# Performance work log

Hardware: AMD Instinct MI355X
Metric: run time of the kernel (lower is better)

## Reference

```python
import jax, jax.numpy as jnp
import numpy as np

N_NODES = 50000
N_EDGES = 800000
IN_FEATS = 32
OUT_FEATS = 64
GRIDSIZE = 8


def setup_inputs() -> dict:
    key = jax.random.key(0)
    k1, k2, k3, k4 = jax.random.split(key, 4)
    x = jax.random.normal(k1, (N_NODES, IN_FEATS), dtype=jnp.float32)
    src = jax.random.randint(k2, (N_EDGES,), 0, N_NODES, dtype=jnp.int32)
    dst = jax.random.randint(k3, (N_EDGES,), 0, N_NODES, dtype=jnp.int32)
    scale = 1.0 / (np.sqrt(IN_FEATS) * np.sqrt(GRIDSIZE))
    fouriercoeffs = jax.random.normal(
        k4, (2, OUT_FEATS, IN_FEATS, GRIDSIZE), dtype=jnp.float32) * scale
    bias = jnp.zeros((OUT_FEATS,), dtype=jnp.float32)
    return {"x": x, "src": src, "dst": dst,
            "fouriercoeffs": fouriercoeffs, "bias": bias}


def reference(x, src, dst, fouriercoeffs, bias):
    # Per-edge source features: [E, in]
    src_feat = x[src]
    # Fourier frequencies k = 1..gridsize: [grid]
    k = jnp.arange(1, GRIDSIZE + 1, dtype=src_feat.dtype)
    # kx: [E, in, grid]
    kx = src_feat[:, :, None] * k[None, None, :]
    cos_kx = jnp.cos(kx)
    sin_kx = jnp.sin(kx)
    # Messages: einsum 'dbik,djik->bj' with d=2 stack of (cos, sin)
    m = (jnp.einsum('eik,jik->ej', cos_kx, fouriercoeffs[0])
         + jnp.einsum('eik,jik->ej', sin_kx, fouriercoeffs[1]))
    # Sum-scatter messages onto destination nodes: [N, out]
    h = jax.ops.segment_sum(m, dst, num_segments=N_NODES)
    return h + bias[None, :]
```

## Files before the change

kernel.cpp:

```cpp
#include <hip/hip_runtime.h>
#include <hip/hip_bf16.h>
#include <math.h>

#define IN_FEATS  32
#define OUT_FEATS 64
#define KDIM      512
#define NPB       64
#define ELLW      64

typedef __attribute__((ext_vector_type(8))) short bf16x8;
typedef __attribute__((ext_vector_type(4))) float f32x4;

static __device__ __forceinline__ unsigned short f2bf(float f) {
    unsigned u = __builtin_bit_cast(unsigned, f);
    return (unsigned short)((u + 0x7fffu + ((u >> 16) & 1u)) >> 16);
}
static __device__ __forceinline__ float bf2f(unsigned short h) {
    return __builtin_bit_cast(float, (unsigned)h << 16);
}

__global__ __launch_bounds__(256) void fkan_node_msg(
    const float* __restrict__ x,
    const float* __restrict__ fc,
    unsigned short* __restrict__ M,
    int* __restrict__ cnt,
    int n_nodes)
{
    __shared__ __align__(16) short phi[NPB * KDIM];
    const int tid  = threadIdx.x;
    const int lane = tid & 63;
    const int wid  = tid >> 6;
    const int nbase = blockIdx.x * NPB;

    if (tid < NPB) {
        const int n = nbase + tid;
        if (n < n_nodes) cnt[n] = 0;
    }

    const int j0   = wid * 16;
    const int brow = j0 + (lane & 15);
    const int kofs = 8 * (lane >> 4);
    bf16x8 bfrag[16];
#pragma unroll
    for (int ks = 0; ks < 16; ++ks) {
        const int K  = ks * 32 + kofs;
        const int b  = K >> 8;
        const int ik = K & 255;
        const float* p = fc + ((size_t)(b * OUT_FEATS + brow) * 256 + ik);
        const float4 f0 = *(const float4*)p;
        const float4 f1 = *(const float4*)(p + 4);
        bf16x8 t;
        t[0] = (short)f2bf(f0.x); t[1] = (short)f2bf(f0.y);
        t[2] = (short)f2bf(f0.z); t[3] = (short)f2bf(f0.w);
        t[4] = (short)f2bf(f1.x); t[5] = (short)f2bf(f1.y);
        t[6] = (short)f2bf(f1.z); t[7] = (short)f2bf(f1.w);
        bfrag[ks] = t;
    }

    {
        const int node = tid >> 2;
        const int q    = tid & 3;
        const int n    = nbase + node;
        char* rowp = (char*)phi + node * 1024;
        const int sw = (node & 7) << 4;
        float xv[8];
        if (n < n_nodes) {
            const float4 a = *(const float4*)(x + (size_t)n * 32 + q * 8);
            const float4 b = *(const float4*)(x + (size_t)n * 32 + q * 8 + 4);
            xv[0]=a.x; xv[1]=a.y; xv[2]=a.z; xv[3]=a.w;
            xv[4]=b.x; xv[5]=b.y; xv[6]=b.z; xv[7]=b.w;
        } else {
#pragma unroll
            for (int u = 0; u < 8; ++u) xv[u] = 0.f;
        }
#pragma unroll
        for (int u = 0; u < 8; ++u) {
            const int i = q * 8 + u;
            const float f  = xv[u] * 0.15915494309189535f;
            const float fr = f - floorf(f);
            const float s1 = __builtin_amdgcn_sinf(fr);
            const float c1 = __builtin_amdgcn_cosf(fr);
            const float twoc = 2.f * c1;
            float cAm = 1.f, sAm = 0.f, cA = c1, sA = s1;
            int pcv[4], psv[4];
#pragma unroll
            for (int p = 0; p < 4; ++p) {
                const float cB = twoc * cA - cAm;
                const float sB = twoc * sA - sAm;
                pcv[p] = (int)(((unsigned)f2bf(cB) << 16) | f2bf(cA));
                psv[p] = (int)(((unsigned)f2bf(sB) << 16) | f2bf(sA));
                const float cN = twoc * cB - cA;
                const float sN = twoc * sB - sA;
                cAm = cB; sAm = sB; cA = cN; sA = sN;
            }
            int4 vc; vc.x = pcv[0]; vc.y = pcv[1]; vc.z = pcv[2]; vc.w = pcv[3];
            int4 vs; vs.x = psv[0]; vs.y = psv[1]; vs.z = psv[2]; vs.w = psv[3];
            *(int4*)(rowp + ((i * 16) ^ sw))       = vc;
            *(int4*)(rowp + ((512 + i * 16) ^ sw)) = vs;
        }
    }
    __syncthreads();

    f32x4 acc[4] = {{0.f,0.f,0.f,0.f},{0.f,0.f,0.f,0.f},
                    {0.f,0.f,0.f,0.f},{0.f,0.f,0.f,0.f}};
    const int arow = lane & 15;
    const int sw   = (arow & 7) << 4;
    const int kbyt = 16 * (lane >> 4);
#pragma unroll
    for (int ks = 0; ks < 16; ++ks) {
#pragma unroll
        for (int nt = 0; nt < 4; ++nt) {
            const int row = nt * 16 + arow;
            const bf16x8 afrag = *(const bf16x8*)
                ((const char*)phi + row * 1024 + ((ks * 64 + kbyt) ^ sw));
            acc[nt] = __builtin_amdgcn_mfma_f32_16x16x32_bf16(
                afrag, bfrag[ks], acc[nt], 0, 0, 0);
        }
    }

    const int rem = n_nodes - nbase;
#pragma unroll
    for (int nt = 0; nt < 4; ++nt) {
        const int rbase = nt * 16 + (lane >> 4) * 4;
#pragma unroll
        for (int r = 0; r < 4; ++r) {
            const int node = rbase + r;
            if (node < rem)
                M[(size_t)(nbase + node) * OUT_FEATS + j0 + (lane & 15)] =
                    f2bf(acc[nt][r]);
        }
    }
}

__global__ __launch_bounds__(256) void fkan_fill(
    const int* __restrict__ src, const int* __restrict__ dst,
    int* __restrict__ cnt, unsigned short* __restrict__ ebuf,
    int n_edges, int n8)
{
    const int r    = blockIdx.x & 7;
    const int slab = blockIdx.x >> 3;
    const int e0   = (slab * 256 + threadIdx.x) * 4;
    if (e0 >= n_edges) return;
    const int lim = r * n8;
    if (e0 + 3 < n_edges) {
        const int4 d4 = *(const int4*)(dst + e0);
        if ((unsigned)(d4.x - lim) < (unsigned)n8) {
            const int pos = atomicAdd(&cnt[d4.x], 1);
            if (pos < ELLW) ebuf[(size_t)d4.x * ELLW + pos] = (unsigned short)src[e0 + 0];
        }
        if ((unsigned)(d4.y - lim) < (unsigned)n8) {
            const int pos = atomicAdd(&cnt[d4.y], 1);
            if (pos < ELLW) ebuf[(size_t)d4.y * ELLW + pos] = (unsigned short)src[e0 + 1];
        }
        if ((unsigned)(d4.z - lim) < (unsigned)n8) {
            const int pos = atomicAdd(&cnt[d4.z], 1);
            if (pos < ELLW) ebuf[(size_t)d4.z * ELLW + pos] = (unsigned short)src[e0 + 2];
        }
        if ((unsigned)(d4.w - lim) < (unsigned)n8) {
            const int pos = atomicAdd(&cnt[d4.w], 1);
            if (pos < ELLW) ebuf[(size_t)d4.w * ELLW + pos] = (unsigned short)src[e0 + 3];
        }
    } else {
        for (int e = e0; e < n_edges; ++e) {
            const int d = dst[e];
            if ((unsigned)(d - lim) < (unsigned)n8) {
                const int pos = atomicAdd(&cnt[d], 1);
                if (pos < ELLW) ebuf[(size_t)d * ELLW + pos] = (unsigned short)src[e];
            }
        }
    }
}

__global__ __launch_bounds__(256) void fkan_gather(
    const int* __restrict__ cnt, const unsigned short* __restrict__ ebuf,
    const unsigned short* __restrict__ M, const float* __restrict__ bias,
    float* __restrict__ out, int n_nodes)
{
    const int tid  = threadIdx.x;
    const int lane = tid & 63;
    const int node = blockIdx.x * 8 + (tid >> 6) * 2 + (lane >> 5);
    if (node >= n_nodes) return;
    const int len = min(cnt[node], ELLW);
    const unsigned short* row = ebuf + (size_t)node * ELLW;
    const int l32  = lane & 31;
    const int sub  = l32 >> 3;
    const int colb = (l32 & 7) * 8;
    float acc[8] = {0.f,0.f,0.f,0.f,0.f,0.f,0.f,0.f};
    const bf16x8 vz = {0,0,0,0,0,0,0,0};
    const unsigned ones = 0x3F803F80u;
    for (int e = 0; e < len; e += 8) {
        const int eeA = e + sub;
        const int eeB = e + 4 + sub;
        const bool pA = eeA < len;
        const bool pB = eeB < len;
        const int sA = pA ? row[eeA] : 0;
        const int sB = pB ? row[eeB] : 0;
        const bf16x8 vA = pA ? *(const bf16x8*)(M + (size_t)sA * OUT_FEATS + colb) : vz;
        const bf16x8 vB = pB ? *(const bf16x8*)(M + (size_t)sB * OUT_FEATS + colb) : vz;
        const uint4 ua = __builtin_bit_cast(uint4, vA);
        const uint4 ub = __builtin_bit_cast(uint4, vB);
        const unsigned uaw[4] = {ua.x, ua.y, ua.z, ua.w};
        const unsigned ubw[4] = {ub.x, ub.y, ub.z, ub.w};
#pragma unroll
        for (int w = 0; w < 4; ++w) {
            const unsigned lo = __builtin_amdgcn_perm(uaw[w], ubw[w], 0x05040100u);
            const unsigned hi = __builtin_amdgcn_perm(uaw[w], ubw[w], 0x07060302u);
            asm("v_dot2_f32_bf16 %0, %1, %2, %0"
                : "+v"(acc[2 * w]) : "v"(lo), "v"(ones));
            asm("v_dot2_f32_bf16 %0, %1, %2, %0"
                : "+v"(acc[2 * w + 1]) : "v"(hi), "v"(ones));
        }
    }
#pragma unroll
    for (int m = 8; m <= 16; m <<= 1) {
#pragma unroll
        for (int c = 0; c < 8; ++c) acc[c] += __shfl_xor(acc[c], m);
    }
    if (sub == 0) {
        const float4 b0 = *(const float4*)(bias + colb);
        const float4 b1 = *(const float4*)(bias + colb + 4);
        float4 o0; o0.x = acc[0] + b0.x; o0.y = acc[1] + b0.y;
                   o0.z = acc[2] + b0.z; o0.w = acc[3] + b0.w;
        float4 o1; o1.x = acc[4] + b1.x; o1.y = acc[5] + b1.y;
                   o1.z = acc[6] + b1.z; o1.w = acc[7] + b1.w;
        *(float4*)(out + (size_t)node * OUT_FEATS + colb)     = o0;
        *(float4*)(out + (size_t)node * OUT_FEATS + colb + 4) = o1;
    }
}

extern "C" void kernel_launch(void* const* d_in, const int* in_sizes, int n_in,
                              void* d_out, int out_size, void* d_ws, size_t ws_size,
                              hipStream_t stream)
{
    const float* x    = (const float*)d_in[0];
    const int*   src  = (const int*)d_in[1];
    const int*   dst  = (const int*)d_in[2];
    const float* fc   = (const float*)d_in[3];
    const float* bias = (const float*)d_in[4];
    float* out = (float*)d_out;

    const int n_nodes = in_sizes[0] / IN_FEATS;
    const int n_edges = in_sizes[1];
    const int n8      = (n_nodes + 7) / 8;

    char* ws = (char*)d_ws;
    unsigned short* M    = (unsigned short*)ws;
    unsigned short* ebuf = (unsigned short*)(ws + (size_t)n_nodes * OUT_FEATS * 2);
    int* cnt = (int*)((char*)ebuf + (size_t)n_nodes * ELLW * 2);

    fkan_node_msg<<<(n_nodes + NPB - 1) / NPB, 256, 0, stream>>>(
        x, fc, M, cnt, n_nodes);

    fkan_fill<<<8 * ((n_edges + 1023) / 1024), 256, 0, stream>>>(
        src, dst, cnt, ebuf, n_edges, n8);

    fkan_gather<<<(n_nodes + 7) / 8, 256, 0, stream>>>(
        cnt, ebuf, M, bias, out, n_nodes);
}
```

Baseline: 88.72 us.

## Fuse node-message and edge-fill kernels into one interleaved launch

Merges the node message-computation kernel and the edge bucketing (fill) kernel into a single launch. Block indices are interleaved so every fifth block computes node messages and the other four run the atomic edge fill, letting compute-heavy MFMA work overlap with atomic/memory-bound fill work. Zeroing of the counters moves to a memset ahead of the kernel, since fill blocks now run concurrently with node blocks. Nodes per block drop from 64 to 32 to balance the interleave ratio. This adds a memset launch and halves MFMA work per block, which reuses the per-block coefficient fragment load over fewer nodes.

```diff
diff --git a/kernel.cpp b/kernel.cpp
--- a/kernel.cpp
+++ b/kernel.cpp
@@ -5,7 +5,7 @@
 #define IN_FEATS  32
 #define OUT_FEATS 64
 #define KDIM      512
-#define NPB       64
+#define NPB       32
 #define ELLW      64
 
 typedef __attribute__((ext_vector_type(8))) short bf16x8;
@@ -19,23 +19,63 @@
     return __builtin_bit_cast(float, (unsigned)h << 16);
 }
 
-__global__ __launch_bounds__(256) void fkan_node_msg(
+__global__ __launch_bounds__(256) void fkan_nmf(
     const float* __restrict__ x,
     const float* __restrict__ fc,
+    const int* __restrict__ src,
+    const int* __restrict__ dst,
     unsigned short* __restrict__ M,
     int* __restrict__ cnt,
-    int n_nodes)
+    unsigned short* __restrict__ ebuf,
+    int n_nodes, int n_edges, int n8, int node_blocks, int fill_blocks)
 {
     __shared__ __align__(16) short phi[NPB * KDIM];
-    const int tid  = threadIdx.x;
-    const int lane = tid & 63;
-    const int wid  = tid >> 6;
-    const int nbase = blockIdx.x * NPB;
-
-    if (tid < NPB) {
-        const int n = nbase + tid;
-        if (n < n_nodes) cnt[n] = 0;
-    }
+    const int b   = blockIdx.x;
+    const int tid = threadIdx.x;
+
+    if (b % 5 != 0) {
+        const int f = b - b / 5 - 1;
+        if (f >= fill_blocks) return;
+        const int r    = f & 7;
+        const int slab = f >> 3;
+        const int e0   = (slab * 256 + tid) * 4;
+        if (e0 >= n_edges) return;
+        const int lim = r * n8;
+        if (e0 + 3 < n_edges) {
+            const int4 d4 = *(const int4*)(dst + e0);
+            if ((unsigned)(d4.x - lim) < (unsigned)n8) {
+                const int pos = atomicAdd(&cnt[d4.x], 1);
+                if (pos < ELLW) ebuf[(size_t)d4.x * ELLW + pos] = (unsigned short)src[e0 + 0];
+            }
+            if ((unsigned)(d4.y - lim) < (unsigned)n8) {
+                const int pos = atomicAdd(&cnt[d4.y], 1);
+                if (pos < ELLW) ebuf[(size_t)d4.y * ELLW + pos] = (unsigned short)src[e0 + 1];
+            }
+            if ((unsigned)(d4.z - lim) < (unsigned)n8) {
+                const int pos = atomicAdd(&cnt[d4.z], 1);
+                if (pos < ELLW) ebuf[(size_t)d4.z * ELLW + pos] = (unsigned short)src[e0 + 2];
+            }
+            if ((unsigned)(d4.w - lim) < (unsigned)n8) {
+                const int pos = atomicAdd(&cnt[d4.w], 1);
+                if (pos < ELLW) ebuf[(size_t)d4.w * ELLW + pos] = (unsigned short)src[e0 + 3];
+            }
+        } else {
+            for (int e = e0; e < n_edges; ++e) {
+                const int d = dst[e];
+                if ((unsigned)(d - lim) < (unsigned)n8) {
+                    const int pos = atomicAdd(&cnt[d], 1);
+                    if (pos < ELLW) ebuf[(size_t)d * ELLW + pos] = (unsigned short)src[e];
+                }
+            }
+        }
+        return;
+    }
+
+    const int nbt = b / 5;
+    if (nbt >= node_blocks) return;
+    const int lane  = tid & 63;
+    const int wid   = tid >> 6;
+    const int nbase = nbt * NPB;
 
     const int j0   = wid * 16;
     const int brow = j0 + (lane & 15);
@@ -44,9 +84,9 @@
 #pragma unroll
     for (int ks = 0; ks < 16; ++ks) {
         const int K  = ks * 32 + kofs;
-        const int b  = K >> 8;
+        const int br = K >> 8;
         const int ik = K & 255;
-        const float* p = fc + ((size_t)(b * OUT_FEATS + brow) * 256 + ik);
+        const float* p = fc + ((size_t)(br * OUT_FEATS + brow) * 256 + ik);
         const float4 f0 = *(const float4*)p;
         const float4 f1 = *(const float4*)(p + 4);
         bf16x8 t;
@@ -58,24 +98,22 @@
     }
 
     {
-        const int node = tid >> 2;
-        const int q    = tid & 3;
+        const int node = tid >> 3;
+        const int q    = tid & 7;
         const int n    = nbase + node;
         char* rowp = (char*)phi + node * 1024;
         const int sw = (node & 7) << 4;
-        float xv[8];
+        float xv[4];
         if (n < n_nodes) {
-            const float4 a = *(const float4*)(x + (size_t)n * 32 + q * 8);
-            const float4 b = *(const float4*)(x + (size_t)n * 32 + q * 8 + 4);
-            xv[0]=a.x; xv[1]=a.y; xv[2]=a.z; xv[3]=a.w;
-            xv[4]=b.x; xv[5]=b.y; xv[6]=b.z; xv[7]=b.w;
+            const float4 a = *(const float4*)(x + (size_t)n * 32 + q * 4);
+            xv[0] = a.x; xv[1] = a.y; xv[2] = a.z; xv[3] = a.w;
         } else {
 #pragma unroll
-            for (int u = 0; u < 8; ++u) xv[u] = 0.f;
-        }
-#pragma unroll
-        for (int u = 0; u < 8; ++u) {
-            const int i = q * 8 + u;
+            for (int u = 0; u < 4; ++u) xv[u] = 0.f;
+        }
+#pragma unroll
+        for (int u = 0; u < 4; ++u) {
+            const int i = q * 4 + u;
             const float f  = xv[u] * 0.15915494309189535f;
             const float fr = f - floorf(f);
             const float s1 = __builtin_amdgcn_sinf(fr);
@@ -101,15 +139,14 @@
     }
     __syncthreads();
 
-    f32x4 acc[4] = {{0.f,0.f,0.f,0.f},{0.f,0.f,0.f,0.f},
-                    {0.f,0.f,0.f,0.f},{0.f,0.f,0.f,0.f}};
+    f32x4 acc[2] = {{0.f,0.f,0.f,0.f},{0.f,0.f,0.f,0.f}};
     const int arow = lane & 15;
     const int sw   = (arow & 7) << 4;
     const int kbyt = 16 * (lane >> 4);
 #pragma unroll
     for (int ks = 0; ks < 16; ++ks) {
 #pragma unroll
-        for (int nt = 0; nt < 4; ++nt) {
+        for (int nt = 0; nt < 2; ++nt) {
             const int row = nt * 16 + arow;
             const bf16x8 afrag = *(const bf16x8*)
                 ((const char*)phi + row * 1024 + ((ks * 64 + kbyt) ^ sw));
@@ -120,7 +157,7 @@
 
     const int rem = n_nodes - nbase;
 #pragma unroll
-    for (int nt = 0; nt < 4; ++nt) {
+    for (int nt = 0; nt < 2; ++nt) {
         const int rbase = nt * 16 + (lane >> 4) * 4;
 #pragma unroll
         for (int r = 0; r < 4; ++r) {
@@ -128,45 +165,6 @@
             if (node < rem)
                 M[(size_t)(nbase + node) * OUT_FEATS + j0 + (lane & 15)] =
                     f2bf(acc[nt][r]);
-        }
-    }
-}
-
-__global__ __launch_bounds__(256) void fkan_fill(
-    const int* __restrict__ src, const int* __restrict__ dst,
-    int* __restrict__ cnt, unsigned short* __restrict__ ebuf,
-    int n_edges, int n8)
-{
-    const int r    = blockIdx.x & 7;
-    const int slab = blockIdx.x >> 3;
-    const int e0   = (slab * 256 + threadIdx.x) * 4;
-    if (e0 >= n_edges) return;
-    const int lim = r * n8;
-    if (e0 + 3 < n_edges) {
-        const int4 d4 = *(const int4*)(dst + e0);
-        if ((unsigned)(d4.x - lim) < (unsigned)n8) {
-            const int pos = atomicAdd(&cnt[d4.x], 1);
-            if (pos < ELLW) ebuf[(size_t)d4.x * ELLW + pos] = (unsigned short)src[e0 + 0];
-        }
-        if ((unsigned)(d4.y - lim) < (unsigned)n8) {
-            const int pos = atomicAdd(&cnt[d4.y], 1);
-            if (pos < ELLW) ebuf[(size_t)d4.y * ELLW + pos] = (unsigned short)src[e0 + 1];
-        }
-        if ((unsigned)(d4.z - lim) < (unsigned)n8) {
-            const int pos = atomicAdd(&cnt[d4.z], 1);
-            if (pos < ELLW) ebuf[(size_t)d4.z * ELLW + pos] = (unsigned short)src[e0 + 2];
-        }
-        if ((unsigned)(d4.w - lim) < (unsigned)n8) {
-            const int pos = atomicAdd(&cnt[d4.w], 1);
-            if (pos < ELLW) ebuf[(size_t)d4.w * ELLW + pos] = (unsigned short)src[e0 + 3];
-        }
-    } else {
-        for (int e = e0; e < n_edges; ++e) {
-            const int d = dst[e];
-            if ((unsigned)(d - lim) < (unsigned)n8) {
-                const int pos = atomicAdd(&cnt[d], 1);
-                if (pos < ELLW) ebuf[(size_t)d * ELLW + pos] = (unsigned short)src[e];
-            }
         }
     }
 }
@@ -243,16 +241,21 @@
     const int n_edges = in_sizes[1];
     const int n8      = (n_nodes + 7) / 8;
 
+    const int node_blocks = (n_nodes + NPB - 1) / NPB;
+    const int fill_blocks = 8 * ((n_edges + 1023) / 1024);
+    const int m = max(node_blocks, (fill_blocks + 3) / 4);
+    const int total_blocks = 5 * m;
+
     char* ws = (char*)d_ws;
     unsigned short* M    = (unsigned short*)ws;
     unsigned short* ebuf = (unsigned short*)(ws + (size_t)n_nodes * OUT_FEATS * 2);
     int* cnt = (int*)((char*)ebuf + (size_t)n_nodes * ELLW * 2);
 
-    fkan_node_msg<<<(n_nodes + NPB - 1) / NPB, 256, 0, stream>>>(
-        x, fc, M, cnt, n_nodes);
-
-    fkan_fill<<<8 * ((n_edges + 1023) / 1024), 256, 0, stream>>>(
-        src, dst, cnt, ebuf, n_edges, n8);
+    hipMemsetAsync(cnt, 0, (size_t)n_nodes * sizeof(int), stream);
+
+    fkan_nmf<<<total_blocks, 256, 0, stream>>>(
+        x, fc, src, dst, M, cnt, ebuf, n_nodes, n_edges, n8,
+        node_blocks, fill_blocks);
 
     fkan_gather<<<(n_nodes + 7) / 8, 256, 0, stream>>>(
         cnt, ebuf, M, bias, out, n_nodes);
```

Result: no change. 88.24 us (-0.5%).
